# Kernel tuning notes

Measured on AMD Instinct MI355X. Metric: run time of the kernel, lower is better.

## Reference

```python
import jax, jax.numpy as jnp
import numpy as np

KV = 128        # key_value_size
EMB = 2 * KV    # embed_dim, tied to output projection
H1 = 512        # decoder_hidden_dim
VOCAB = 30


def _lstm_cell(x, h, c, Wih, Whh, bih, bhh):
    # torch LSTMCell gate order: input, forget, cell(g), output
    gates = x @ Wih.T + bih + h @ Whh.T + bhh
    i, f, g, o = jnp.split(gates, 4, axis=-1)
    c_new = jax.nn.sigmoid(f) * c + jax.nn.sigmoid(i) * jnp.tanh(g)
    h_new = jax.nn.sigmoid(o) * jnp.tanh(c_new)
    return h_new, c_new


def setup_inputs() -> dict:
    key = jax.random.key(0)
    ks = jax.random.split(key, 16)
    B, T, L = 128, 512, 256
    s = 0.05
    inp = {
        "key": jax.random.normal(ks[0], (B, T, KV), jnp.float32),
        "value": jax.random.normal(ks[1], (B, T, KV), jnp.float32),
        "encoder_len": jax.random.randint(ks[2], (B,), 1, T + 1),
        "y": jax.random.randint(ks[3], (B, L), 0, VOCAB),
        "emb_W": jax.random.normal(ks[4], (VOCAB, EMB), jnp.float32) * s,
        "W_ih1": jax.random.normal(ks[5], (4 * H1, EMB + KV), jnp.float32) * s,
        "W_hh1": jax.random.normal(ks[6], (4 * H1, H1), jnp.float32) * s,
        "b_ih1": jax.random.normal(ks[7], (4 * H1,), jnp.float32) * s,
        "b_hh1": jax.random.normal(ks[8], (4 * H1,), jnp.float32) * s,
        "W_ih2": jax.random.normal(ks[9], (4 * KV, H1), jnp.float32) * s,
        "W_hh2": jax.random.normal(ks[10], (4 * KV, KV), jnp.float32) * s,
        "b_ih2": jax.random.normal(ks[11], (4 * KV,), jnp.float32) * s,
        "b_hh2": jax.random.normal(ks[12], (4 * KV,), jnp.float32) * s,
        "out_b": jax.random.normal(ks[13], (VOCAB,), jnp.float32) * s,
    }
    return inp


def reference(key, value, encoder_len, y, emb_W, W_ih1, W_hh1, b_ih1, b_hh1,
              W_ih2, W_hh2, b_ih2, b_hh2, out_b):
    B, T, _ = key.shape
    L = y.shape[1]
    scale = 1.0 / jnp.sqrt(jnp.asarray(KV, key.dtype))

    # padding mask over encoder timesteps: True = masked
    mask = jnp.arange(T)[None, :] >= encoder_len[:, None]  # (B, T)

    # teacher forcing with rate 1.0: input at t is embedding(y[:, t-1]), zeros at t=0
    char_embeddings = emb_W[y]  # (B, L, EMB)
    char_in = jnp.concatenate(
        [jnp.zeros((B, 1, EMB), emb_W.dtype), char_embeddings[:, :-1]], axis=1)
    char_in = jnp.transpose(char_in, (1, 0, 2))  # (L, B, EMB)

    h1 = jnp.zeros((B, H1), key.dtype)
    c1 = jnp.zeros((B, H1), key.dtype)
    h2 = jnp.zeros((B, KV), key.dtype)
    c2 = jnp.zeros((B, KV), key.dtype)
    ctx = jnp.zeros((B, KV), key.dtype)

    def step(carry, ce):
        h1, c1, h2, c2, ctx = carry
        x = jnp.concatenate([ce, ctx], axis=1)
        h1, c1 = _lstm_cell(x, h1, c1, W_ih1, W_hh1, b_ih1, b_hh1)
        h2, c2 = _lstm_cell(h1, h2, c2, W_ih2, W_hh2, b_ih2, b_hh2)
        q = h2  # (B, KV)
        energy = jnp.einsum('btd,bd->bt', key, q)
        energy = jnp.where(mask, -1e9, energy)
        attn = jax.nn.softmax(energy * scale, axis=1)  # (B, T)
        ctx_new = jnp.einsum('bt,btd->bd', attn, value)  # (B, KV)
        pred = jnp.concatenate([q, ctx_new], axis=1) @ emb_W.T + out_b
        return (h1, c1, h2, c2, ctx_new), (pred, attn[0])

    _, (preds, attn0) = jax.lax.scan(step, (h1, c1, h2, c2, ctx), char_in)
    predictions = jnp.transpose(preds, (1, 0, 2))  # (B, L, VOCAB)
    attentions = attn0  # (L, T) -- attention of batch element 0 per step
    return predictions, attentions
```

## Files before the change

kernel.cpp:

```cpp
#include <hip/hip_runtime.h>

#define B_   128
#define T_   512
#define KV_  128
#define H1_  512
#define L_   256
#define NVOC 30
#define NPRED (B_*L_*NVOC)
#define NTHR 512

typedef __attribute__((ext_vector_type(8))) short short8v;
typedef __attribute__((ext_vector_type(4))) float float4v;

__device__ __forceinline__ float bf2f(unsigned short u) {
  union { unsigned int u; float f; } c; c.u = ((unsigned int)u) << 16; return c.f;
}
__device__ __forceinline__ unsigned short f2bf(float f) {
  union { float f; unsigned int u; } c; c.f = f;
  unsigned int r = (c.u + 0x7fffu + ((c.u >> 16) & 1u)) >> 16;
  return (unsigned short)r;
}
__device__ __forceinline__ unsigned int packhl(float x) {
  unsigned short hi = f2bf(x);
  unsigned short lo = f2bf(x - bf2f(hi));
  return (unsigned int)hi | ((unsigned int)lo << 16);
}
__device__ __forceinline__ float sigm(float x) { return 1.0f / (1.0f + __expf(-x)); }
__device__ __forceinline__ float tanhh(float x) { return 1.0f - 2.0f / (1.0f + __expf(2.0f * x)); }

__device__ __forceinline__ unsigned int aloadu(const unsigned int* p) {
  return __hip_atomic_load((unsigned int*)p, __ATOMIC_RELAXED, __HIP_MEMORY_SCOPE_AGENT);
}
__device__ __forceinline__ void astoreu(unsigned int* p, unsigned int v) {
  __hip_atomic_store(p, v, __ATOMIC_RELAXED, __HIP_MEMORY_SCOPE_AGENT);
}
__device__ __forceinline__ float4v mfma16(short8v a, short8v b, float4v c) {
  return __builtin_amdgcn_mfma_f32_16x16x32_bf16(a, b, c, 0, 0, 0);
}

struct DecParams {
  const int* y; const int* enc_len;
  const float* W_ih1; const float* W_hh1;
  const float* W_ih2; const float* W_hh2;
  const float* b_ih2; const float* b_hh2;
  const float* table; const unsigned int* keyRM; const float* value;
  unsigned int* H1hi; unsigned int* H1lo;
  unsigned int* H2hi; unsigned int* H2lo;
  unsigned int* CTXhi; unsigned int* CTXlo;
  float* qstore; float* ctxstore; float* attn_out;
  int* flags;
};

__global__ void prep_kernel(const float* __restrict__ key,
                            const float* __restrict__ emb_W, const float* __restrict__ W_ih1,
                            const float* __restrict__ b_ih1, const float* __restrict__ b_hh1,
                            float* __restrict__ table, unsigned int* __restrict__ keyRM,
                            float* __restrict__ zbase) {
  const int NT_TAB = 31 * 2048;
  const int NT_KEY = B_ * T_ * 64;
  const int NT_ZER = 2*(2*B_*256) + 2*(2*B_*64) + 2*(B_*64) + 384;
  const int total = NT_TAB + NT_KEY + NT_ZER;
  for (int i = blockIdx.x * blockDim.x + threadIdx.x; i < total;
       i += gridDim.x * blockDim.x) {
    if (i < NT_TAB) {
      int row = i & 2047, v = i >> 11;
      float acc = b_ih1[row] + b_hh1[row];
      if (v < NVOC) {
        const float* e = emb_W + v * 256;
        const float* w = W_ih1 + row * 384;
        #pragma unroll 4
        for (int k = 0; k < 256; ++k) acc += e[k] * w[k];
      }
      table[v * 2048 + row] = acc;
    } else if (i < NT_TAB + NT_KEY) {
      int j = i - NT_TAB;
      int dp = j & 63, r = j >> 6;
      int tt = r & 511, b = r >> 9;
      int src = (b * T_ + tt) * KV_ + 2 * dp;
      unsigned int lo = f2bf(key[src]), hi = f2bf(key[src + 1]);
      keyRM[(r << 6) + (dp ^ ((tt & 7) << 2))] = lo | (hi << 16);
    } else {
      zbase[i - NT_TAB - NT_KEY] = 0.0f;
    }
  }
}

__global__ void __launch_bounds__(NTHR) decoder_main(DecParams P) {
  __shared__ __align__(16) unsigned char smem[145664];
  const int blk = blockIdx.x, tid = threadIdx.x;
  const int lane = tid & 63, w = tid >> 6;
  const int lr = lane & 15, lk = lane >> 4;

  if (blk < B_) {
    float* e_as = (float*)(smem + 131072);
    unsigned int* a_hl = (unsigned int*)(smem + 133120);
    float* red  = (float*)(smem + 135168);
    const int b = blk, g32 = b & ~31;

    { const uint4* src = (const uint4*)(P.keyRM + (size_t)b * (T_ * 64));
      uint4* dst = (uint4*)smem;
      for (int i = tid; i < (T_ * 64) / 4; i += NTHR) dst[i] = src[i]; }
    short8v vfragv[16];
    { const float* vb = P.value + (size_t)b * T_ * KV_ + (w * 16 + lr);
      #pragma unroll
      for (int ks = 0; ks < 16; ++ks) {
        union { unsigned short us[8]; short8v s; } tv;
        #pragma unroll
        for (int j = 0; j < 8; ++j) tv.us[j] = f2bf(vb[(ks * 32 + lk * 8 + j) * KV_]);
        vfragv[ks] = tv.s;
      } }
    const int len = P.enc_len[b];
    const float SCALE = 0.08838834764831845f;
    __syncthreads();

    for (int t = 0; t < L_; ++t) {
      const int np = (t & 1) ^ 1;
      if (tid < 64) {
        const int idx = 256 + g32 + (tid & 31);
        while (true) {
          int v = __hip_atomic_load(&P.flags[idx], __ATOMIC_RELAXED, __HIP_MEMORY_SCOPE_AGENT);
          if (__all(v >= t + 1)) break;
          __builtin_amdgcn_s_sleep(1);
        }
      }
      __syncthreads();
      union frag_t { unsigned int u[4]; short8v s; };
      frag_t qh[4], ql[4];
      { const unsigned int* Hh = P.H2hi + np * (B_ * 64) + b * 64;
        const unsigned int* Hl = P.H2lo + np * (B_ * 64) + b * 64;
        #pragma unroll
        for (int ks = 0; ks < 4; ++ks)
          #pragma unroll
          for (int jj = 0; jj < 4; ++jj) {
            qh[ks].u[jj] = aloadu(Hh + ks * 16 + lk * 4 + jj);
            ql[ks].u[jj] = aloadu(Hl + ks * 16 + lk * 4 + jj);
          } }
      #pragma unroll
      for (int i = 0; i < 4; ++i) {
        const int t0 = (w * 4 + i) * 16;
        const int tloc = t0 + lr;
        const unsigned char* rowp = smem + tloc * 256;
        const int sw = (tloc & 7) << 4;
        float4v acc = {0.0f, 0.0f, 0.0f, 0.0f};
        #pragma unroll
        for (int ks = 0; ks < 4; ++ks) {
          short8v av = *(const short8v*)(rowp + ((ks * 64 + lk * 16) ^ sw));
          acc = mfma16(av, qh[ks].s, acc);
          acc = mfma16(av, ql[ks].s, acc);
        }
        if (lr == 0) {
          #pragma unroll
          for (int j2 = 0; j2 < 4; ++j2) e_as[t0 + lk * 4 + j2] = acc[j2];
        }
      }
      __syncthreads();
      float e = (tid < len) ? e_as[tid] * SCALE : -8.8388348e7f;
      float m = e;
      #pragma unroll
      for (int off = 32; off > 0; off >>= 1) m = fmaxf(m, __shfl_xor(m, off));
      if (lane == 0) red[w] = m;
      __syncthreads();
      float M = red[0];
      #pragma unroll
      for (int i2 = 1; i2 < 8; ++i2) M = fmaxf(M, red[i2]);
      float pe = __expf(e - M);
      float s = pe;
      #pragma unroll
      for (int off = 32; off > 0; off >>= 1) s += __shfl_xor(s, off);
      if (lane == 0) red[8 + w] = s;
      a_hl[tid] = packhl(pe);
      __syncthreads();
      float S = 0.0f;
      #pragma unroll
      for (int i2 = 0; i2 < 8; ++i2) S += red[8 + i2];
      const float invS = 1.0f / S;
      float4v acc0 = {0.0f, 0.0f, 0.0f, 0.0f};
      float4v acc1 = {0.0f, 0.0f, 0.0f, 0.0f};
      #pragma unroll
      for (int ks = 0; ks < 16; ++ks) {
        const unsigned int* ap = a_hl + ks * 32 + lk * 8;
        uint4 ua = *(const uint4*)(ap);
        uint4 ub = *(const uint4*)(ap + 4);
        union { unsigned short us[8]; short8v s; } ah, al;
        ah.us[0] = (unsigned short)ua.x;  al.us[0] = (unsigned short)(ua.x >> 16);
        ah.us[1] = (unsigned short)ua.y;  al.us[1] = (unsigned short)(ua.y >> 16);
        ah.us[2] = (unsigned short)ua.z;  al.us[2] = (unsigned short)(ua.z >> 16);
        ah.us[3] = (unsigned short)ua.w;  al.us[3] = (unsigned short)(ua.w >> 16);
        ah.us[4] = (unsigned short)ub.x;  al.us[4] = (unsigned short)(ub.x >> 16);
        ah.us[5] = (unsigned short)ub.y;  al.us[5] = (unsigned short)(ub.y >> 16);
        ah.us[6] = (unsigned short)ub.z;  al.us[6] = (unsigned short)(ub.z >> 16);
        ah.us[7] = (unsigned short)ub.w;  al.us[7] = (unsigned short)(ub.w >> 16);
        acc0 = mfma16(ah.s, vfragv[ks], acc0);
        acc1 = mfma16(al.s, vfragv[ks], acc1);
      }
      float cv = (acc0[0] + acc1[0]) * invS;
      float cvp = __shfl_xor(cv, 1);
      if (lane < 16) {
        const int d = w * 16 + lane;
        P.ctxstore[((size_t)t * B_ + b) * KV_ + d] = cv;
        if (!(lane & 1)) {
          unsigned short h0 = f2bf(cv),  l0 = f2bf(cv - bf2f(h0));
          unsigned short h1v = f2bf(cvp), l1 = f2bf(cvp - bf2f(h1v));
          astoreu(&P.CTXhi[b * 64 + (d >> 1)], (unsigned int)h0 | ((unsigned int)h1v << 16));
          astoreu(&P.CTXlo[b * 64 + (d >> 1)], (unsigned int)l0 | ((unsigned int)l1 << 16));
        }
      }
      if (b == 0) P.attn_out[t * T_ + tid] = pe * invS;
      __syncthreads();
      if (tid == 0)
        __hip_atomic_store(&P.flags[128 + b], t + 1, __ATOMIC_RELAXED, __HIP_MEMORY_SCOPE_AGENT);
    }
  } else {
    unsigned short* W1l = (unsigned short*)smem;
    unsigned short* W2l = (unsigned short*)(smem + 82944);
    unsigned short* xT  = (unsigned short*)(smem + 103680);
    unsigned int*   xTu = (unsigned int*)(smem + 103680);
    float* gbuf = (float*)(smem + 136960);
    const int lb = blk - B_;
    const int ds = lb & 31, g32 = (lb >> 5) << 5;

    for (int idx = tid; idx < 64 * 640; idx += NTHR) {
      int r = idx / 640, k = idx - r * 640;
      int grow = (r & 3) * 512 + ds * 16 + (r >> 2);
      float wv = (k < 128) ? P.W_ih1[grow * 384 + 256 + k]
                           : P.W_hh1[grow * 512 + (k - 128)];
      W1l[r * 648 + k] = f2bf(wv);
    }
    for (int idx = tid; idx < 16 * 640; idx += NTHR) {
      int r = idx / 640, k = idx - r * 640;
      int grow = (r & 3) * 128 + ds * 4 + (r >> 2);
      float wv = (k < 512) ? P.W_ih2[grow * 512 + k]
                           : P.W_hh2[grow * 128 + (k - 512)];
      W2l[r * 648 + k] = f2bf(wv);
    }
    float c1 = 0.0f;
    float c2 = 0.0f;
    float bi2[4];
    {
      const int dloc = tid & 3;
      #pragma unroll
      for (int gq = 0; gq < 4; ++gq) {
        const int grow = gq * 128 + ds * 4 + dloc;
        bi2[gq] = P.b_ih2[grow] + P.b_hh2[grow];
      }
    }
    __syncthreads();

    const int mt = w & 1, nt = w >> 1;

    for (int t = 0; t < L_; ++t) {
      const int p = t & 1, np = p ^ 1;
      if (tid < 64) {
        const int idx = (tid < 32) ? (g32 + tid) : (256 + g32 + (tid - 32));
        while (true) {
          int v = __hip_atomic_load(&P.flags[idx], __ATOMIC_RELAXED, __HIP_MEMORY_SCOPE_AGENT);
          if (__all(v >= t)) break;
          __builtin_amdgcn_s_sleep(1);
        }
      }
      __syncthreads();

      unsigned int rh[16], rl[16];
      {
        const unsigned int* Sh = P.H1hi + p * (B_ * 256);
        const unsigned int* Sl = P.H1lo + p * (B_ * 256);
        #pragma unroll
        for (int ii = 0; ii < 16; ++ii) {
          int i = tid + ii * NTHR; int bq = i >> 8, kp = i & 255;
          int off = (g32 + bq) * 256 + kp;
          rh[ii] = aloadu(Sh + off);
          rl[ii] = aloadu(Sl + off);
        }
      }

      float4v acc2 = {0.0f, 0.0f, 0.0f, 0.0f};
      if (w < 2) {
        const int arow = (g32 + w * 16 + lr) * 64 + lk * 4;
        const unsigned int* Sh = P.H2hi + p * (B_ * 64) + arow;
        const unsigned int* Sl = P.H2lo + p * (B_ * 64) + arow;
        #pragma unroll
        for (int ks = 0; ks < 4; ++ks) {
          union { unsigned int u[4]; short8v s; } ah, al;
          #pragma unroll
          for (int j = 0; j < 4; ++j) { ah.u[j] = aloadu(Sh + ks * 16 + j);
                                        al.u[j] = aloadu(Sl + ks * 16 + j); }
          short8v bv = *(const short8v*)(W2l + lr * 648 + 512 + lk * 8 + ks * 32);
          acc2 = mfma16(ah.s, bv, acc2);
          acc2 = mfma16(al.s, bv, acc2);
        }
      }

      float4v acc1 = {0.0f, 0.0f, 0.0f, 0.0f};
      #pragma unroll
      for (int ii = 0; ii < 16; ++ii) {
        int i = tid + ii * NTHR; xTu[(i >> 8) * 260 + (i & 255)] = rh[ii];
      }
      __syncthreads();
      {
        const unsigned short* ap = xT + (mt * 16 + lr) * 520 + lk * 8;
        const unsigned short* bp = W1l + (nt * 16 + lr) * 648 + 128 + lk * 8;
        #pragma unroll
        for (int ks = 0; ks < 16; ++ks)
          acc1 = mfma16(*(const short8v*)(ap + ks * 32),
                        *(const short8v*)(bp + ks * 32), acc1);
      }
      __syncthreads();
      #pragma unroll
      for (int ii = 0; ii < 16; ++ii) {
        int i = tid + ii * NTHR; xTu[(i >> 8) * 260 + (i & 255)] = rl[ii];
      }
      __syncthreads();
      {
        const unsigned short* ap = xT + (mt * 16 + lr) * 520 + lk * 8;
        const unsigned short* bp = W1l + (nt * 16 + lr) * 648 + 128 + lk * 8;
        #pragma unroll
        for (int ks = 0; ks < 16; ++ks)
          acc1 = mfma16(*(const short8v*)(ap + ks * 32),
                        *(const short8v*)(bp + ks * 32), acc1);
      }

      if (tid < 64) {
        const int idx = 128 + g32 + (tid & 31);
        while (true) {
          int v = __hip_atomic_load(&P.flags[idx], __ATOMIC_RELAXED, __HIP_MEMORY_SCOPE_AGENT);
          if (__all(v >= t)) break;
          __builtin_amdgcn_s_sleep(1);
        }
      }
      __syncthreads();
      {
        const int arow = (g32 + mt * 16 + lr) * 64 + lk * 4;
        const unsigned int* Sh = P.CTXhi + arow;
        const unsigned int* Sl = P.CTXlo + arow;
        #pragma unroll
        for (int ks = 0; ks < 4; ++ks) {
          union { unsigned int u[4]; short8v s; } ah, al;
          #pragma unroll
          for (int j = 0; j < 4; ++j) { ah.u[j] = aloadu(Sh + ks * 16 + j);
                                        al.u[j] = aloadu(Sl + ks * 16 + j); }
          short8v bv = *(const short8v*)(W1l + (nt * 16 + lr) * 648 + lk * 8 + ks * 32);
          acc1 = mfma16(ah.s, bv, acc1);
          acc1 = mfma16(al.s, bv, acc1);
        }
      }
      {
        const int m0 = mt * 16 + lk * 4, n = nt * 16 + lr;
        #pragma unroll
        for (int j = 0; j < 4; ++j) gbuf[(m0 + j) * 68 + n] = acc1[j];
      }
      __syncthreads();
      {
        const int bq = tid >> 4, d = tid & 15, gb = g32 + bq;
        float4 gv = *(const float4*)&gbuf[bq * 68 + 4 * d];
        const int ci = (t == 0) ? NVOC : P.y[gb * L_ + (t - 1)];
        const int dg = ds * 16 + d;
        const float* tb = P.table + ci * 2048 + dg;
        float gi = gv.x + tb[0];
        float gf = gv.y + tb[512];
        float gg = gv.z + tb[1024];
        float go = gv.w + tb[1536];
        float cn = sigm(gf) * c1 + sigm(gi) * tanhh(gg);
        float hn = sigm(go) * tanhh(cn);
        c1 = cn;
        float hnp = __shfl_xor(hn, 1);
        if (!(d & 1)) {
          unsigned short h0 = f2bf(hn),  l0 = f2bf(hn - bf2f(h0));
          unsigned short h1v = f2bf(hnp), l1 = f2bf(hnp - bf2f(h1v));
          astoreu(&P.H1hi[np * (B_ * 256) + gb * 256 + ds * 8 + (d >> 1)],
                  (unsigned int)h0 | ((unsigned int)h1v << 16));
          astoreu(&P.H1lo[np * (B_ * 256) + gb * 256 + ds * 8 + (d >> 1)],
                  (unsigned int)l0 | ((unsigned int)l1 << 16));
        }
      }
      __syncthreads();
      if (tid == 0)
        __hip_atomic_store(&P.flags[lb], t + 1, __ATOMIC_RELAXED, __HIP_MEMORY_SCOPE_AGENT);
      if (tid < 64) {
        const int idx = g32 + (tid & 31);
        while (true) {
          int v = __hip_atomic_load(&P.flags[idx], __ATOMIC_RELAXED, __HIP_MEMORY_SCOPE_AGENT);
          if (__all(v >= t + 1)) break;
          __builtin_amdgcn_s_sleep(1);
        }
      }
      __syncthreads();
      {
        const unsigned int* Sh = P.H1hi + np * (B_ * 256);
        const unsigned int* Sl = P.H1lo + np * (B_ * 256);
        #pragma unroll
        for (int ii = 0; ii < 16; ++ii) {
          int i = tid + ii * NTHR; int bq = i >> 8, kp = i & 255;
          int off = (g32 + bq) * 256 + kp;
          rh[ii] = aloadu(Sh + off);
          rl[ii] = aloadu(Sl + off);
        }
      }
      #pragma unroll
      for (int ii = 0; ii < 16; ++ii) {
        int i = tid + ii * NTHR; xTu[(i >> 8) * 260 + (i & 255)] = rh[ii];
      }
      __syncthreads();
      if (w < 2) {
        const unsigned short* ap = xT + (w * 16 + lr) * 520 + lk * 8;
        const unsigned short* bp = W2l + lr * 648 + lk * 8;
        #pragma unroll
        for (int ks = 0; ks < 16; ++ks)
          acc2 = mfma16(*(const short8v*)(ap + ks * 32),
                        *(const short8v*)(bp + ks * 32), acc2);
      }
      __syncthreads();
      #pragma unroll
      for (int ii = 0; ii < 16; ++ii) {
        int i = tid + ii * NTHR; xTu[(i >> 8) * 260 + (i & 255)] = rl[ii];
      }
      __syncthreads();
      if (w < 2) {
        const unsigned short* ap = xT + (w * 16 + lr) * 520 + lk * 8;
        const unsigned short* bp = W2l + lr * 648 + lk * 8;
        #pragma unroll
        for (int ks = 0; ks < 16; ++ks)
          acc2 = mfma16(*(const short8v*)(ap + ks * 32),
                        *(const short8v*)(bp + ks * 32), acc2);
        const int m0 = w * 16 + lk * 4, n = lr;
        #pragma unroll
        for (int j = 0; j < 4; ++j) gbuf[(m0 + j) * 68 + n] = acc2[j];
      }
      __syncthreads();
      if (tid < 128) {
        const int bq = tid >> 2, dloc = tid & 3, gb = g32 + bq;
        float4 gv = *(const float4*)&gbuf[bq * 68 + 4 * dloc];
        float gi = gv.x + bi2[0];
        float gf = gv.y + bi2[1];
        float gg = gv.z + bi2[2];
        float go = gv.w + bi2[3];
        float cn = sigm(gf) * c2 + sigm(gi) * tanhh(gg);
        float hn = sigm(go) * tanhh(cn);
        c2 = cn;
        P.qstore[((size_t)t * B_ + gb) * KV_ + ds * 4 + dloc] = hn;
        float hnp = __shfl_xor(hn, 1);
        if (!(dloc & 1)) {
          unsigned short h0 = f2bf(hn),  l0 = f2bf(hn - bf2f(h0));
          unsigned short h1v = f2bf(hnp), l1 = f2bf(hnp - bf2f(h1v));
          astoreu(&P.H2hi[np * (B_ * 64) + gb * 64 + ds * 2 + (dloc >> 1)],
                  (unsigned int)h0 | ((unsigned int)h1v << 16));
          astoreu(&P.H2lo[np * (B_ * 64) + gb * 64 + ds * 2 + (dloc >> 1)],
                  (unsigned int)l0 | ((unsigned int)l1 << 16));
        }
      }
      __syncthreads();
      if (tid == 0)
        __hip_atomic_store(&P.flags[256 + lb], t + 1, __ATOMIC_RELAXED, __HIP_MEMORY_SCOPE_AGENT);
    }
  }
}

__global__ void pred_tail(const float* __restrict__ qstore, const float* __restrict__ ctxstore,
                          const float* __restrict__ emb_W, const float* __restrict__ out_b,
                          float* __restrict__ preds) {
  int o = blockIdx.x * 256 + threadIdx.x;
  if (o >= NPRED) return;
  int v = o % NVOC;
  int bt = o / NVOC;
  int b = bt >> 8, t = bt & 255;
  const float* q  = qstore   + ((size_t)t * B_ + b) * KV_;
  const float* cx = ctxstore + ((size_t)t * B_ + b) * KV_;
  const float* er = emb_W + v * 256;
  float acc = out_b[v];
  #pragma unroll 4
  for (int e = 0; e < 128; ++e) acc += q[e] * er[e] + cx[e] * er[128 + e];
  preds[o] = acc;
}

extern "C" void kernel_launch(void* const* d_in, const int* in_sizes, int n_in,
                              void* d_out, int out_size, void* d_ws, size_t ws_size,
                              hipStream_t stream) {
  const float* key    = (const float*)d_in[0];
  const float* value  = (const float*)d_in[1];
  const int*   enclen = (const int*)d_in[2];
  const int*   y      = (const int*)d_in[3];
  const float* emb_W  = (const float*)d_in[4];
  const float* W_ih1  = (const float*)d_in[5];
  const float* W_hh1  = (const float*)d_in[6];
  const float* b_ih1  = (const float*)d_in[7];
  const float* b_hh1  = (const float*)d_in[8];
  const float* W_ih2  = (const float*)d_in[9];
  const float* W_hh2  = (const float*)d_in[10];
  const float* b_ih2  = (const float*)d_in[11];
  const float* b_hh2  = (const float*)d_in[12];
  const float* out_b  = (const float*)d_in[13];

  float* f = (float*)d_ws;
  float* table = f;                        f += 31 * 2048;
  unsigned int* keyRM = (unsigned int*)f;  f += B_ * T_ * 64;
  unsigned int* H1hi = (unsigned int*)f;   f += 2 * B_ * 256;
  unsigned int* H1lo = (unsigned int*)f;   f += 2 * B_ * 256;
  unsigned int* H2hi = (unsigned int*)f;   f += 2 * B_ * 64;
  unsigned int* H2lo = (unsigned int*)f;   f += 2 * B_ * 64;
  unsigned int* CTXhi = (unsigned int*)f;  f += B_ * 64;
  unsigned int* CTXlo = (unsigned int*)f;  f += B_ * 64;
  int*   flags = (int*)f;                  f += 384;
  float* qstore   = f;                     f += (size_t)L_ * B_ * KV_;
  float* ctxstore = f;                     f += (size_t)L_ * B_ * KV_;

  float* preds    = (float*)d_out;
  float* attn_out = preds + NPRED;

  prep_kernel<<<4096, 256, 0, stream>>>(key, emb_W, W_ih1, b_ih1, b_hh1,
                                        table, keyRM, (float*)H1hi);

  DecParams P{ y, enclen, W_ih1, W_hh1, W_ih2, W_hh2, b_ih2, b_hh2,
               table, keyRM, value, H1hi, H1lo, H2hi, H2lo, CTXhi, CTXlo,
               qstore, ctxstore, attn_out, flags };
  void* kargs[] = { (void*)&P };
  hipLaunchCooperativeKernel((void*)decoder_main, dim3(256), dim3(NTHR), kargs, 0, stream);

  pred_tail<<<(NPRED + 255) / 256, 256, 0, stream>>>(qstore, ctxstore, emb_W, out_b, preds);
}
```

Baseline: 4.797 ms.

## Replace per-block flag barriers with step-tagged 64-bit data words for H2/CTX exchange

The H2 and CTX words exchanged between the attention blocks and the LSTM blocks now carry a 32-bit step tag in their upper half. Consumers spin directly on the tagged data instead of waiting on separate flag arrays behind __syncthreads, which removes a flag store/load round trip and several block barriers per timestep. The LSTM2 input path also loads H1 hi/lo straight from global memory into MFMA operands instead of staging them through shared memory with extra barriers. In exchange, the exchanged buffers double in size and every wave spins with no sleep, which adds memory polling traffic.

```diff
diff --git a/kernel.cpp b/kernel.cpp
--- a/kernel.cpp
+++ b/kernel.cpp
@@ -20,11 +20,6 @@
   unsigned int r = (c.u + 0x7fffu + ((c.u >> 16) & 1u)) >> 16;
   return (unsigned short)r;
 }
-__device__ __forceinline__ unsigned int packhl(float x) {
-  unsigned short hi = f2bf(x);
-  unsigned short lo = f2bf(x - bf2f(hi));
-  return (unsigned int)hi | ((unsigned int)lo << 16);
-}
 __device__ __forceinline__ float sigm(float x) { return 1.0f / (1.0f + __expf(-x)); }
 __device__ __forceinline__ float tanhh(float x) { return 1.0f - 2.0f / (1.0f + __expf(2.0f * x)); }
 
@@ -32,6 +27,12 @@
   return __hip_atomic_load((unsigned int*)p, __ATOMIC_RELAXED, __HIP_MEMORY_SCOPE_AGENT);
 }
 __device__ __forceinline__ void astoreu(unsigned int* p, unsigned int v) {
+  __hip_atomic_store(p, v, __ATOMIC_RELAXED, __HIP_MEMORY_SCOPE_AGENT);
+}
+__device__ __forceinline__ unsigned long long aloadu64(const unsigned long long* p) {
+  return __hip_atomic_load((unsigned long long*)p, __ATOMIC_RELAXED, __HIP_MEMORY_SCOPE_AGENT);
+}
+__device__ __forceinline__ void astoreu64(unsigned long long* p, unsigned long long v) {
   __hip_atomic_store(p, v, __ATOMIC_RELAXED, __HIP_MEMORY_SCOPE_AGENT);
 }
 __device__ __forceinline__ float4v mfma16(short8v a, short8v b, float4v c) {
@@ -45,8 +46,10 @@
   const float* b_ih2; const float* b_hh2;
   const float* table; const unsigned int* keyRM; const float* value;
   unsigned int* H1hi; unsigned int* H1lo;
-  unsigned int* H2hi; unsigned int* H2lo;
-  unsigned int* CTXhi; unsigned int* CTXlo;
+  unsigned long long* H2hi64;
+  unsigned long long* H2lo64;
+  unsigned long long* CTXhi64;
+  unsigned long long* CTXlo64;
   float* qstore; float* ctxstore; float* attn_out;
   int* flags;
 };
@@ -58,7 +61,7 @@
                             float* __restrict__ zbase) {
   const int NT_TAB = 31 * 2048;
   const int NT_KEY = B_ * T_ * 64;
-  const int NT_ZER = 2*(2*B_*256) + 2*(2*B_*64) + 2*(B_*64) + 384;
+  const int NT_ZER = 2 * 65536 + 2 * 32768 + 2 * 16384 + 384;
   const int total = NT_TAB + NT_KEY + NT_ZER;
   for (int i = blockIdx.x * blockDim.x + threadIdx.x; i < total;
        i += gridDim.x * blockDim.x) {
@@ -95,7 +98,7 @@
     float* e_as = (float*)(smem + 131072);
     unsigned int* a_hl = (unsigned int*)(smem + 133120);
     float* red  = (float*)(smem + 135168);
-    const int b = blk, g32 = b & ~31;
+    const int b = blk;
 
     { const uint4* src = (const uint4*)(P.keyRM + (size_t)b * (T_ * 64));
       uint4* dst = (uint4*)smem;
@@ -115,26 +118,38 @@
 
     for (int t = 0; t < L_; ++t) {
       const int np = (t & 1) ^ 1;
-      if (tid < 64) {
-        const int idx = 256 + g32 + (tid & 31);
-        while (true) {
-          int v = __hip_atomic_load(&P.flags[idx], __ATOMIC_RELAXED, __HIP_MEMORY_SCOPE_AGENT);
-          if (__all(v >= t + 1)) break;
-          __builtin_amdgcn_s_sleep(1);
-        }
-      }
-      __syncthreads();
       union frag_t { unsigned int u[4]; short8v s; };
       frag_t qh[4], ql[4];
-      { const unsigned int* Hh = P.H2hi + np * (B_ * 64) + b * 64;
-        const unsigned int* Hl = P.H2lo + np * (B_ * 64) + b * 64;
+      {
+        const unsigned long long* Qh = P.H2hi64 + np * (B_ * 64) + b * 64;
+        const unsigned long long* Ql = P.H2lo64 + np * (B_ * 64) + b * 64;
+        const unsigned int want = (unsigned int)(t + 1);
+        while ((unsigned int)(aloadu64(Qh + lk * 4) >> 32) != want) {}
+        unsigned long long vh[16], vl[16];
+        bool okall;
+        do {
+          #pragma unroll
+          for (int ks = 0; ks < 4; ++ks)
+            #pragma unroll
+            for (int j = 0; j < 4; ++j) {
+              vh[ks * 4 + j] = aloadu64(Qh + ks * 16 + lk * 4 + j);
+              vl[ks * 4 + j] = aloadu64(Ql + ks * 16 + lk * 4 + j);
+            }
+          bool ok = true;
+          #pragma unroll
+          for (int ii = 0; ii < 16; ++ii)
+            ok = ok && ((unsigned int)(vh[ii] >> 32) == want)
+                    && ((unsigned int)(vl[ii] >> 32) == want);
+          okall = __all(ok);
+        } while (!okall);
         #pragma unroll
         for (int ks = 0; ks < 4; ++ks)
           #pragma unroll
-          for (int jj = 0; jj < 4; ++jj) {
-            qh[ks].u[jj] = aloadu(Hh + ks * 16 + lk * 4 + jj);
-            ql[ks].u[jj] = aloadu(Hl + ks * 16 + lk * 4 + jj);
-          } }
+          for (int j = 0; j < 4; ++j) {
+            qh[ks].u[j] = (unsigned int)vh[ks * 4 + j];
+            ql[ks].u[j] = (unsigned int)vl[ks * 4 + j];
+          }
+      }
       #pragma unroll
       for (int i = 0; i < 4; ++i) {
         const int t0 = (w * 4 + i) * 16;
@@ -168,7 +183,11 @@
       #pragma unroll
       for (int off = 32; off > 0; off >>= 1) s += __shfl_xor(s, off);
       if (lane == 0) red[8 + w] = s;
-      a_hl[tid] = packhl(pe);
+      {
+        unsigned short hi = f2bf(pe);
+        unsigned short lo = f2bf(pe - bf2f(hi));
+        a_hl[tid] = (unsigned int)hi | ((unsigned int)lo << 16);
+      }
       __syncthreads();
       float S = 0.0f;
       #pragma unroll
@@ -201,14 +220,14 @@
         if (!(lane & 1)) {
           unsigned short h0 = f2bf(cv),  l0 = f2bf(cv - bf2f(h0));
           unsigned short h1v = f2bf(cvp), l1 = f2bf(cvp - bf2f(h1v));
-          astoreu(&P.CTXhi[b * 64 + (d >> 1)], (unsigned int)h0 | ((unsigned int)h1v << 16));
-          astoreu(&P.CTXlo[b * 64 + (d >> 1)], (unsigned int)l0 | ((unsigned int)l1 << 16));
+          unsigned long long g = ((unsigned long long)(t + 1)) << 32;
+          astoreu64(&P.CTXhi64[b * 64 + (d >> 1)],
+                    g | (unsigned long long)((unsigned int)h0 | ((unsigned int)h1v << 16)));
+          astoreu64(&P.CTXlo64[b * 64 + (d >> 1)],
+                    g | (unsigned long long)((unsigned int)l0 | ((unsigned int)l1 << 16)));
         }
       }
       if (b == 0) P.attn_out[t * T_ + tid] = pe * invS;
-      __syncthreads();
-      if (tid == 0)
-        __hip_atomic_store(&P.flags[128 + b], t + 1, __ATOMIC_RELAXED, __HIP_MEMORY_SCOPE_AGENT);
     }
   } else {
     unsigned short* W1l = (unsigned short*)smem;
@@ -251,7 +270,7 @@
     for (int t = 0; t < L_; ++t) {
       const int p = t & 1, np = p ^ 1;
       if (tid < 64) {
-        const int idx = (tid < 32) ? (g32 + tid) : (256 + g32 + (tid - 32));
+        const int idx = g32 + (tid & 31);
         while (true) {
           int v = __hip_atomic_load(&P.flags[idx], __ATOMIC_RELAXED, __HIP_MEMORY_SCOPE_AGENT);
           if (__all(v >= t)) break;
@@ -276,14 +295,33 @@
       float4v acc2 = {0.0f, 0.0f, 0.0f, 0.0f};
       if (w < 2) {
         const int arow = (g32 + w * 16 + lr) * 64 + lk * 4;
-        const unsigned int* Sh = P.H2hi + p * (B_ * 64) + arow;
-        const unsigned int* Sl = P.H2lo + p * (B_ * 64) + arow;
+        const unsigned long long* Sh = P.H2hi64 + p * (B_ * 64) + arow;
+        const unsigned long long* Sl = P.H2lo64 + p * (B_ * 64) + arow;
+        const unsigned int want = (unsigned int)t;
+        while ((unsigned int)(aloadu64(Sh) >> 32) != want) {}
+        unsigned long long vh[16], vl[16];
+        bool okall;
+        do {
+          #pragma unroll
+          for (int ks = 0; ks < 4; ++ks)
+            #pragma unroll
+            for (int j = 0; j < 4; ++j) {
+              vh[ks * 4 + j] = aloadu64(Sh + ks * 16 + j);
+              vl[ks * 4 + j] = aloadu64(Sl + ks * 16 + j);
+            }
+          bool ok = true;
+          #pragma unroll
+          for (int ii = 0; ii < 16; ++ii)
+            ok = ok && ((unsigned int)(vh[ii] >> 32) == want)
+                    && ((unsigned int)(vl[ii] >> 32) == want);
+          okall = __all(ok);
+        } while (!okall);
         #pragma unroll
         for (int ks = 0; ks < 4; ++ks) {
           union { unsigned int u[4]; short8v s; } ah, al;
           #pragma unroll
-          for (int j = 0; j < 4; ++j) { ah.u[j] = aloadu(Sh + ks * 16 + j);
-                                        al.u[j] = aloadu(Sl + ks * 16 + j); }
+          for (int j = 0; j < 4; ++j) { ah.u[j] = (unsigned int)vh[ks * 4 + j];
+                                        al.u[j] = (unsigned int)vl[ks * 4 + j]; }
           short8v bv = *(const short8v*)(W2l + lr * 648 + 512 + lk * 8 + ks * 32);
           acc2 = mfma16(ah.s, bv, acc2);
           acc2 = mfma16(al.s, bv, acc2);
@@ -319,25 +357,35 @@
                         *(const short8v*)(bp + ks * 32), acc1);
       }
 
-      if (tid < 64) {
-        const int idx = 128 + g32 + (tid & 31);
-        while (true) {
-          int v = __hip_atomic_load(&P.flags[idx], __ATOMIC_RELAXED, __HIP_MEMORY_SCOPE_AGENT);
-          if (__all(v >= t)) break;
-          __builtin_amdgcn_s_sleep(1);
-        }
-      }
-      __syncthreads();
       {
         const int arow = (g32 + mt * 16 + lr) * 64 + lk * 4;
-        const unsigned int* Sh = P.CTXhi + arow;
-        const unsigned int* Sl = P.CTXlo + arow;
+        const unsigned long long* Ch = P.CTXhi64 + arow;
+        const unsigned long long* Cl = P.CTXlo64 + arow;
+        const unsigned int want = (unsigned int)t;
+        while ((unsigned int)(aloadu64(Ch) >> 32) != want) {}
+        unsigned long long vh[16], vl[16];
+        bool okall;
+        do {
+          #pragma unroll
+          for (int ks = 0; ks < 4; ++ks)
+            #pragma unroll
+            for (int j = 0; j < 4; ++j) {
+              vh[ks * 4 + j] = aloadu64(Ch + ks * 16 + j);
+              vl[ks * 4 + j] = aloadu64(Cl + ks * 16 + j);
+            }
+          bool ok = true;
+          #pragma unroll
+          for (int ii = 0; ii < 16; ++ii)
+            ok = ok && ((unsigned int)(vh[ii] >> 32) == want)
+                    && ((unsigned int)(vl[ii] >> 32) == want);
+          okall = __all(ok);
+        } while (!okall);
         #pragma unroll
         for (int ks = 0; ks < 4; ++ks) {
           union { unsigned int u[4]; short8v s; } ah, al;
           #pragma unroll
-          for (int j = 0; j < 4; ++j) { ah.u[j] = aloadu(Sh + ks * 16 + j);
-                                        al.u[j] = aloadu(Sl + ks * 16 + j); }
+          for (int j = 0; j < 4; ++j) { ah.u[j] = (unsigned int)vh[ks * 4 + j];
+                                        al.u[j] = (unsigned int)vl[ks * 4 + j]; }
           short8v bv = *(const short8v*)(W1l + (nt * 16 + lr) * 648 + lk * 8 + ks * 32);
           acc1 = mfma16(ah.s, bv, acc1);
           acc1 = mfma16(al.s, bv, acc1);
@@ -384,43 +432,27 @@
         }
       }
       __syncthreads();
-      {
-        const unsigned int* Sh = P.H1hi + np * (B_ * 256);
-        const unsigned int* Sl = P.H1lo + np * (B_ * 256);
-        #pragma unroll
-        for (int ii = 0; ii < 16; ++ii) {
-          int i = tid + ii * NTHR; int bq = i >> 8, kp = i & 255;
-          int off = (g32 + bq) * 256 + kp;
-          rh[ii] = aloadu(Sh + off);
-          rl[ii] = aloadu(Sl + off);
-        }
-      }
-      #pragma unroll
-      for (int ii = 0; ii < 16; ++ii) {
-        int i = tid + ii * NTHR; xTu[(i >> 8) * 260 + (i & 255)] = rh[ii];
-      }
-      __syncthreads();
       if (w < 2) {
-        const unsigned short* ap = xT + (w * 16 + lr) * 520 + lk * 8;
-        const unsigned short* bp = W2l + lr * 648 + lk * 8;
+        const unsigned int* Sh = P.H1hi + np * (B_ * 256) + (g32 + w * 16 + lr) * 256 + lk * 4;
+        const unsigned int* Sl = P.H1lo + np * (B_ * 256) + (g32 + w * 16 + lr) * 256 + lk * 4;
+        unsigned int gh[64], gl[64];
         #pragma unroll
         for (int ks = 0; ks < 16; ++ks)
-          acc2 = mfma16(*(const short8v*)(ap + ks * 32),
-                        *(const short8v*)(bp + ks * 32), acc2);
-      }
-      __syncthreads();
-      #pragma unroll
-      for (int ii = 0; ii < 16; ++ii) {
-        int i = tid + ii * NTHR; xTu[(i >> 8) * 260 + (i & 255)] = rl[ii];
-      }
-      __syncthreads();
-      if (w < 2) {
-        const unsigned short* ap = xT + (w * 16 + lr) * 520 + lk * 8;
-        const unsigned short* bp = W2l + lr * 648 + lk * 8;
-        #pragma unroll
-        for (int ks = 0; ks < 16; ++ks)
-          acc2 = mfma16(*(const short8v*)(ap + ks * 32),
-                        *(const short8v*)(bp + ks * 32), acc2);
+          #pragma unroll
+          for (int j = 0; j < 4; ++j) {
+            gh[ks * 4 + j] = aloadu(Sh + ks * 16 + j);
+            gl[ks * 4 + j] = aloadu(Sl + ks * 16 + j);
+          }
+        #pragma unroll
+        for (int ks = 0; ks < 16; ++ks) {
+          union { unsigned int u[4]; short8v s; } ah, al;
+          #pragma unroll
+          for (int j = 0; j < 4; ++j) { ah.u[j] = gh[ks * 4 + j];
+                                        al.u[j] = gl[ks * 4 + j]; }
+          short8v bv = *(const short8v*)(W2l + lr * 648 + lk * 8 + ks * 32);
+          acc2 = mfma16(ah.s, bv, acc2);
+          acc2 = mfma16(al.s, bv, acc2);
+        }
         const int m0 = w * 16 + lk * 4, n = lr;
         #pragma unroll
         for (int j = 0; j < 4; ++j) gbuf[(m0 + j) * 68 + n] = acc2[j];
@@ -441,15 +473,13 @@
         if (!(dloc & 1)) {
           unsigned short h0 = f2bf(hn),  l0 = f2bf(hn - bf2f(h0));
           unsigned short h1v = f2bf(hnp), l1 = f2bf(hnp - bf2f(h1v));
-          astoreu(&P.H2hi[np * (B_ * 64) + gb * 64 + ds * 2 + (dloc >> 1)],
-                  (unsigned int)h0 | ((unsigned int)h1v << 16));
-          astoreu(&P.H2lo[np * (B_ * 64) + gb * 64 + ds * 2 + (dloc >> 1)],
-                  (unsigned int)l0 | ((unsigned int)l1 << 16));
-        }
-      }
-      __syncthreads();
-      if (tid == 0)
-        __hip_atomic_store(&P.flags[256 + lb], t + 1, __ATOMIC_RELAXED, __HIP_MEMORY_SCOPE_AGENT);
+          unsigned long long g = ((unsigned long long)(t + 1)) << 32;
+          astoreu64(&P.H2hi64[np * (B_ * 64) + gb * 64 + ds * 2 + (dloc >> 1)],
+                    g | (unsigned long long)((unsigned int)h0 | ((unsigned int)h1v << 16)));
+          astoreu64(&P.H2lo64[np * (B_ * 64) + gb * 64 + ds * 2 + (dloc >> 1)],
+                    g | (unsigned long long)((unsigned int)l0 | ((unsigned int)l1 << 16)));
+        }
+      }
     }
   }
 }
@@ -490,17 +520,17 @@
   const float* out_b  = (const float*)d_in[13];
 
   float* f = (float*)d_ws;
-  float* table = f;                        f += 31 * 2048;
-  unsigned int* keyRM = (unsigned int*)f;  f += B_ * T_ * 64;
-  unsigned int* H1hi = (unsigned int*)f;   f += 2 * B_ * 256;
-  unsigned int* H1lo = (unsigned int*)f;   f += 2 * B_ * 256;
-  unsigned int* H2hi = (unsigned int*)f;   f += 2 * B_ * 64;
-  unsigned int* H2lo = (unsigned int*)f;   f += 2 * B_ * 64;
-  unsigned int* CTXhi = (unsigned int*)f;  f += B_ * 64;
-  unsigned int* CTXlo = (unsigned int*)f;  f += B_ * 64;
-  int*   flags = (int*)f;                  f += 384;
-  float* qstore   = f;                     f += (size_t)L_ * B_ * KV_;
-  float* ctxstore = f;                     f += (size_t)L_ * B_ * KV_;
+  float* table = f;                            f += 31 * 2048;
+  unsigned int* keyRM = (unsigned int*)f;      f += B_ * T_ * 64;
+  unsigned int* H1hi = (unsigned int*)f;       f += 2 * B_ * 256;
+  unsigned int* H1lo = (unsigned int*)f;       f += 2 * B_ * 256;
+  unsigned long long* H2hi64 = (unsigned long long*)f;  f += 2 * (2 * B_ * 64);
+  unsigned long long* H2lo64 = (unsigned long long*)f;  f += 2 * (2 * B_ * 64);
+  unsigned long long* CTXhi64 = (unsigned long long*)f; f += 2 * (B_ * 64);
+  unsigned long long* CTXlo64 = (unsigned long long*)f; f += 2 * (B_ * 64);
+  int*   flags = (int*)f;                      f += 384;
+  float* qstore   = f;                         f += (size_t)L_ * B_ * KV_;
+  float* ctxstore = f;                         f += (size_t)L_ * B_ * KV_;
 
   float* preds    = (float*)d_out;
   float* attn_out = preds + NPRED;
@@ -509,7 +539,7 @@
                                         table, keyRM, (float*)H1hi);
 
   DecParams P{ y, enclen, W_ih1, W_hh1, W_ih2, W_hh2, b_ih2, b_hh2,
-               table, keyRM, value, H1hi, H1lo, H2hi, H2lo, CTXhi, CTXlo,
+               table, keyRM, value, H1hi, H1lo, H2hi64, H2lo64, CTXhi64, CTXlo64,
                qstore, ctxstore, attn_out, flags };
   void* kargs[] = { (void*)&P };
   hipLaunchCooperativeKernel((void*)decoder_main, dim3(256), dim3(NTHR), kargs, 0, stream);
```

After: 6.185 ms. +28.9%, slower.

## Split LSTM2 flag into per-wave flags and drop block-wide barriers in decoder loop

Applied to the files above, without the earlier changes.

Polling of inter-block flags is now done by every wave instead of a single wave followed by __syncthreads, which removes several block barriers per step. The second LSTM cell is computed by only two waves, which load H1 straight from global into registers, and each wave publishes its own flag (256/384 slots). Meanwhile the other waves stage H1 into shared memory for the first LSTM. The goal is to shorten the serial per-timestep critical path across cooperating blocks. The cost is extra polling traffic, a larger flag array, and more register pressure, and the relaxed-ordering correctness now depends on an explicit s_waitcnt before each flag store.

```diff
diff --git a/kernel.cpp b/kernel.cpp
--- a/kernel.cpp
+++ b/kernel.cpp
@@ -19,11 +19,6 @@
   union { float f; unsigned int u; } c; c.f = f;
   unsigned int r = (c.u + 0x7fffu + ((c.u >> 16) & 1u)) >> 16;
   return (unsigned short)r;
-}
-__device__ __forceinline__ unsigned int packhl(float x) {
-  unsigned short hi = f2bf(x);
-  unsigned short lo = f2bf(x - bf2f(hi));
-  return (unsigned int)hi | ((unsigned int)lo << 16);
 }
 __device__ __forceinline__ float sigm(float x) { return 1.0f / (1.0f + __expf(-x)); }
 __device__ __forceinline__ float tanhh(float x) { return 1.0f - 2.0f / (1.0f + __expf(2.0f * x)); }
@@ -58,7 +53,7 @@
                             float* __restrict__ zbase) {
   const int NT_TAB = 31 * 2048;
   const int NT_KEY = B_ * T_ * 64;
-  const int NT_ZER = 2*(2*B_*256) + 2*(2*B_*64) + 2*(B_*64) + 384;
+  const int NT_ZER = 2 * 65536 + 2 * 16384 + 2 * 8192 + 512;
   const int total = NT_TAB + NT_KEY + NT_ZER;
   for (int i = blockIdx.x * blockDim.x + threadIdx.x; i < total;
        i += gridDim.x * blockDim.x) {
@@ -115,15 +110,14 @@
 
     for (int t = 0; t < L_; ++t) {
       const int np = (t & 1) ^ 1;
-      if (tid < 64) {
-        const int idx = 256 + g32 + (tid & 31);
+      {
+        const int idx = (lane < 32) ? (256 + g32 + lane) : (384 + g32 + (lane - 32));
         while (true) {
           int v = __hip_atomic_load(&P.flags[idx], __ATOMIC_RELAXED, __HIP_MEMORY_SCOPE_AGENT);
           if (__all(v >= t + 1)) break;
           __builtin_amdgcn_s_sleep(1);
         }
       }
-      __syncthreads();
       union frag_t { unsigned int u[4]; short8v s; };
       frag_t qh[4], ql[4];
       { const unsigned int* Hh = P.H2hi + np * (B_ * 64) + b * 64;
@@ -153,7 +147,6 @@
           for (int j2 = 0; j2 < 4; ++j2) e_as[t0 + lk * 4 + j2] = acc[j2];
         }
       }
-      __syncthreads();
       float e = (tid < len) ? e_as[tid] * SCALE : -8.8388348e7f;
       float m = e;
       #pragma unroll
@@ -168,7 +161,11 @@
       #pragma unroll
       for (int off = 32; off > 0; off >>= 1) s += __shfl_xor(s, off);
       if (lane == 0) red[8 + w] = s;
-      a_hl[tid] = packhl(pe);
+      {
+        unsigned short hi = f2bf(pe);
+        unsigned short lo = f2bf(pe - bf2f(hi));
+        a_hl[tid] = (unsigned int)hi | ((unsigned int)lo << 16);
+      }
       __syncthreads();
       float S = 0.0f;
       #pragma unroll
@@ -247,34 +244,47 @@
     __syncthreads();
 
     const int mt = w & 1, nt = w >> 1;
+    const int wt = tid - 128;
 
     for (int t = 0; t < L_; ++t) {
       const int p = t & 1, np = p ^ 1;
-      if (tid < 64) {
-        const int idx = (tid < 32) ? (g32 + tid) : (256 + g32 + (tid - 32));
+      {
+        const int idx = g32 + (lane & 31);
         while (true) {
           int v = __hip_atomic_load(&P.flags[idx], __ATOMIC_RELAXED, __HIP_MEMORY_SCOPE_AGENT);
           if (__all(v >= t)) break;
           __builtin_amdgcn_s_sleep(1);
         }
       }
-      __syncthreads();
-
-      unsigned int rh[16], rl[16];
-      {
+
+      unsigned int rh[22], rl[22];
+      float4v acc2 = {0.0f, 0.0f, 0.0f, 0.0f};
+      if (w >= 2) {
         const unsigned int* Sh = P.H1hi + p * (B_ * 256);
         const unsigned int* Sl = P.H1lo + p * (B_ * 256);
         #pragma unroll
-        for (int ii = 0; ii < 16; ++ii) {
-          int i = tid + ii * NTHR; int bq = i >> 8, kp = i & 255;
-          int off = (g32 + bq) * 256 + kp;
-          rh[ii] = aloadu(Sh + off);
-          rl[ii] = aloadu(Sl + off);
-        }
-      }
-
-      float4v acc2 = {0.0f, 0.0f, 0.0f, 0.0f};
-      if (w < 2) {
+        for (int ii = 0; ii < 22; ++ii) {
+          int i = wt + ii * 384;
+          if (i < 8192) {
+            int off = (g32 + (i >> 8)) * 256 + (i & 255);
+            rh[ii] = aloadu(Sh + off);
+            rl[ii] = aloadu(Sl + off);
+          }
+        }
+        #pragma unroll
+        for (int ii = 0; ii < 22; ++ii) {
+          int i = wt + ii * 384;
+          if (i < 8192) xTu[(i >> 8) * 260 + (i & 255)] = rh[ii];
+        }
+      } else {
+        {
+          const int idx = (lane < 32) ? (256 + g32 + lane) : (384 + g32 + (lane - 32));
+          while (true) {
+            int v = __hip_atomic_load(&P.flags[idx], __ATOMIC_RELAXED, __HIP_MEMORY_SCOPE_AGENT);
+            if (__all(v >= t)) break;
+            __builtin_amdgcn_s_sleep(1);
+          }
+        }
         const int arow = (g32 + w * 16 + lr) * 64 + lk * 4;
         const unsigned int* Sh = P.H2hi + p * (B_ * 64) + arow;
         const unsigned int* Sl = P.H2lo + p * (B_ * 64) + arow;
@@ -289,13 +299,8 @@
           acc2 = mfma16(al.s, bv, acc2);
         }
       }
-
+      __syncthreads();
       float4v acc1 = {0.0f, 0.0f, 0.0f, 0.0f};
-      #pragma unroll
-      for (int ii = 0; ii < 16; ++ii) {
-        int i = tid + ii * NTHR; xTu[(i >> 8) * 260 + (i & 255)] = rh[ii];
-      }
-      __syncthreads();
       {
         const unsigned short* ap = xT + (mt * 16 + lr) * 520 + lk * 8;
         const unsigned short* bp = W1l + (nt * 16 + lr) * 648 + 128 + lk * 8;
@@ -305,9 +310,12 @@
                         *(const short8v*)(bp + ks * 32), acc1);
       }
       __syncthreads();
-      #pragma unroll
-      for (int ii = 0; ii < 16; ++ii) {
-        int i = tid + ii * NTHR; xTu[(i >> 8) * 260 + (i & 255)] = rl[ii];
+      if (w >= 2) {
+        #pragma unroll
+        for (int ii = 0; ii < 22; ++ii) {
+          int i = wt + ii * 384;
+          if (i < 8192) xTu[(i >> 8) * 260 + (i & 255)] = rl[ii];
+        }
       }
       __syncthreads();
       {
@@ -319,15 +327,14 @@
                         *(const short8v*)(bp + ks * 32), acc1);
       }
 
-      if (tid < 64) {
-        const int idx = 128 + g32 + (tid & 31);
+      {
+        const int idx = 128 + g32 + (lane & 31);
         while (true) {
           int v = __hip_atomic_load(&P.flags[idx], __ATOMIC_RELAXED, __HIP_MEMORY_SCOPE_AGENT);
           if (__all(v >= t)) break;
           __builtin_amdgcn_s_sleep(1);
         }
       }
-      __syncthreads();
       {
         const int arow = (g32 + mt * 16 + lr) * 64 + lk * 4;
         const unsigned int* Sh = P.CTXhi + arow;
@@ -375,81 +382,67 @@
       __syncthreads();
       if (tid == 0)
         __hip_atomic_store(&P.flags[lb], t + 1, __ATOMIC_RELAXED, __HIP_MEMORY_SCOPE_AGENT);
-      if (tid < 64) {
-        const int idx = g32 + (tid & 31);
-        while (true) {
-          int v = __hip_atomic_load(&P.flags[idx], __ATOMIC_RELAXED, __HIP_MEMORY_SCOPE_AGENT);
-          if (__all(v >= t + 1)) break;
-          __builtin_amdgcn_s_sleep(1);
-        }
-      }
-      __syncthreads();
-      {
-        const unsigned int* Sh = P.H1hi + np * (B_ * 256);
-        const unsigned int* Sl = P.H1lo + np * (B_ * 256);
-        #pragma unroll
-        for (int ii = 0; ii < 16; ++ii) {
-          int i = tid + ii * NTHR; int bq = i >> 8, kp = i & 255;
-          int off = (g32 + bq) * 256 + kp;
-          rh[ii] = aloadu(Sh + off);
-          rl[ii] = aloadu(Sl + off);
-        }
-      }
-      #pragma unroll
-      for (int ii = 0; ii < 16; ++ii) {
-        int i = tid + ii * NTHR; xTu[(i >> 8) * 260 + (i & 255)] = rh[ii];
-      }
-      __syncthreads();
+
       if (w < 2) {
-        const unsigned short* ap = xT + (w * 16 + lr) * 520 + lk * 8;
-        const unsigned short* bp = W2l + lr * 648 + lk * 8;
+        {
+          const int idx = g32 + (lane & 31);
+          while (true) {
+            int v = __hip_atomic_load(&P.flags[idx], __ATOMIC_RELAXED, __HIP_MEMORY_SCOPE_AGENT);
+            if (__all(v >= t + 1)) break;
+            __builtin_amdgcn_s_sleep(1);
+          }
+        }
+        const unsigned int* Sh = P.H1hi + np * (B_ * 256) + (g32 + w * 16 + lr) * 256 + lk * 4;
+        const unsigned int* Sl = P.H1lo + np * (B_ * 256) + (g32 + w * 16 + lr) * 256 + lk * 4;
+        unsigned int gh[64], gl[64];
         #pragma unroll
         for (int ks = 0; ks < 16; ++ks)
-          acc2 = mfma16(*(const short8v*)(ap + ks * 32),
-                        *(const short8v*)(bp + ks * 32), acc2);
-      }
-      __syncthreads();
-      #pragma unroll
-      for (int ii = 0; ii < 16; ++ii) {
-        int i = tid + ii * NTHR; xTu[(i >> 8) * 260 + (i & 255)] = rl[ii];
-      }
-      __syncthreads();
-      if (w < 2) {
-        const unsigned short* ap = xT + (w * 16 + lr) * 520 + lk * 8;
-        const unsigned short* bp = W2l + lr * 648 + lk * 8;
-        #pragma unroll
-        for (int ks = 0; ks < 16; ++ks)
-          acc2 = mfma16(*(const short8v*)(ap + ks * 32),
-                        *(const short8v*)(bp + ks * 32), acc2);
-        const int m0 = w * 16 + lk * 4, n = lr;
-        #pragma unroll
-        for (int j = 0; j < 4; ++j) gbuf[(m0 + j) * 68 + n] = acc2[j];
-      }
-      __syncthreads();
-      if (tid < 128) {
-        const int bq = tid >> 2, dloc = tid & 3, gb = g32 + bq;
-        float4 gv = *(const float4*)&gbuf[bq * 68 + 4 * dloc];
-        float gi = gv.x + bi2[0];
-        float gf = gv.y + bi2[1];
-        float gg = gv.z + bi2[2];
-        float go = gv.w + bi2[3];
-        float cn = sigm(gf) * c2 + sigm(gi) * tanhh(gg);
-        float hn = sigm(go) * tanhh(cn);
-        c2 = cn;
-        P.qstore[((size_t)t * B_ + gb) * KV_ + ds * 4 + dloc] = hn;
-        float hnp = __shfl_xor(hn, 1);
-        if (!(dloc & 1)) {
-          unsigned short h0 = f2bf(hn),  l0 = f2bf(hn - bf2f(h0));
-          unsigned short h1v = f2bf(hnp), l1 = f2bf(hnp - bf2f(h1v));
-          astoreu(&P.H2hi[np * (B_ * 64) + gb * 64 + ds * 2 + (dloc >> 1)],
-                  (unsigned int)h0 | ((unsigned int)h1v << 16));
-          astoreu(&P.H2lo[np * (B_ * 64) + gb * 64 + ds * 2 + (dloc >> 1)],
-                  (unsigned int)l0 | ((unsigned int)l1 << 16));
-        }
-      }
-      __syncthreads();
-      if (tid == 0)
-        __hip_atomic_store(&P.flags[256 + lb], t + 1, __ATOMIC_RELAXED, __HIP_MEMORY_SCOPE_AGENT);
+          #pragma unroll
+          for (int j = 0; j < 4; ++j) {
+            gh[ks * 4 + j] = aloadu(Sh + ks * 16 + j);
+            gl[ks * 4 + j] = aloadu(Sl + ks * 16 + j);
+          }
+        #pragma unroll
+        for (int ks = 0; ks < 16; ++ks) {
+          union { unsigned int u[4]; short8v s; } ah, al;
+          #pragma unroll
+          for (int j = 0; j < 4; ++j) { ah.u[j] = gh[ks * 4 + j];
+                                        al.u[j] = gl[ks * 4 + j]; }
+          short8v bv = *(const short8v*)(W2l + lr * 648 + lk * 8 + ks * 32);
+          acc2 = mfma16(ah.s, bv, acc2);
+          acc2 = mfma16(al.s, bv, acc2);
+        }
+        {
+          const int m0 = w * 16 + lk * 4, n = lr;
+          #pragma unroll
+          for (int j = 0; j < 4; ++j) gbuf[(m0 + j) * 68 + n] = acc2[j];
+        }
+        {
+          const int bq = tid >> 2, dloc = tid & 3, gb = g32 + bq;
+          float4 gv = *(const float4*)&gbuf[bq * 68 + 4 * dloc];
+          float gi = gv.x + bi2[0];
+          float gf = gv.y + bi2[1];
+          float gg = gv.z + bi2[2];
+          float go = gv.w + bi2[3];
+          float cn = sigm(gf) * c2 + sigm(gi) * tanhh(gg);
+          float hn = sigm(go) * tanhh(cn);
+          c2 = cn;
+          P.qstore[((size_t)t * B_ + gb) * KV_ + ds * 4 + dloc] = hn;
+          float hnp = __shfl_xor(hn, 1);
+          if (!(dloc & 1)) {
+            unsigned short h0 = f2bf(hn),  l0 = f2bf(hn - bf2f(h0));
+            unsigned short h1v = f2bf(hnp), l1 = f2bf(hnp - bf2f(h1v));
+            astoreu(&P.H2hi[np * (B_ * 64) + gb * 64 + ds * 2 + (dloc >> 1)],
+                    (unsigned int)h0 | ((unsigned int)h1v << 16));
+            astoreu(&P.H2lo[np * (B_ * 64) + gb * 64 + ds * 2 + (dloc >> 1)],
+                    (unsigned int)l0 | ((unsigned int)l1 << 16));
+          }
+        }
+        asm volatile("s_waitcnt vmcnt(0)" ::: "memory");
+        if (lane == 0)
+          __hip_atomic_store(&P.flags[(w ? 384 : 256) + lb], t + 1,
+                             __ATOMIC_RELAXED, __HIP_MEMORY_SCOPE_AGENT);
+      }
     }
   }
 }
@@ -498,7 +491,7 @@
   unsigned int* H2lo = (unsigned int*)f;   f += 2 * B_ * 64;
   unsigned int* CTXhi = (unsigned int*)f;  f += B_ * 64;
   unsigned int* CTXlo = (unsigned int*)f;  f += B_ * 64;
-  int*   flags = (int*)f;                  f += 384;
+  int*   flags = (int*)f;                  f += 512;
   float* qstore   = f;                     f += (size_t)L_ * B_ * KV_;
   float* ctxstore = f;                     f += (size_t)L_ * B_ * KV_;
 
```

New measurement: 8.170 ms. +70.3%, slower.
